# Kernel tuning notes

Measured on AMD Instinct MI355X. Metric: run time of the kernel, lower is better.

The kernel has to match this reference:

```python
import jax, jax.numpy as jnp
import numpy as np

N_NODES = 50000
N_EDGES = 1600000
IN_CH = 128
HEADS = 4
OUT_PER_HEAD = 32  # out_channels // heads with concat=True
NEG_SLOPE = 0.2    # GATConv default leaky_relu slope
SOFTMAX_EPS = 1e-16  # PyG scatter-softmax denominator eps
LN_EPS = 1e-5


def setup_inputs() -> dict:
    key = jax.random.key(0)
    ks = jax.random.split(key, 8)
    x = jax.random.normal(ks[0], (N_NODES, IN_CH), dtype=jnp.float32)
    edge_index = jax.random.randint(ks[1], (2, N_EDGES), 0, N_NODES, dtype=jnp.int32)
    W = jax.random.normal(ks[2], (IN_CH, HEADS * OUT_PER_HEAD), dtype=jnp.float32) * (1.0 / np.sqrt(IN_CH))
    att_src = jax.random.normal(ks[3], (HEADS, OUT_PER_HEAD), dtype=jnp.float32) * 0.1
    att_dst = jax.random.normal(ks[4], (HEADS, OUT_PER_HEAD), dtype=jnp.float32) * 0.1
    bias = jnp.zeros((HEADS * OUT_PER_HEAD,), dtype=jnp.float32)
    gamma = jnp.ones((HEADS * OUT_PER_HEAD,), dtype=jnp.float32)
    beta = jnp.zeros((HEADS * OUT_PER_HEAD,), dtype=jnp.float32)
    return {"x": x, "edge_index": edge_index, "W": W, "att_src": att_src,
            "att_dst": att_dst, "bias": bias, "gamma": gamma, "beta": beta}


def reference(x, edge_index, W, att_src, att_dst, bias, gamma, beta):
    N = x.shape[0]
    H, C = att_src.shape
    # GATConv default add_self_loops=True
    loop = jnp.arange(N, dtype=edge_index.dtype)
    src = jnp.concatenate([edge_index[0], loop])  # message source j
    dst = jnp.concatenate([edge_index[1], loop])  # aggregation target i

    h = (x @ W).reshape(N, H, C)                      # [N,H,C]
    a_s = jnp.einsum('nhc,hc->nh', h, att_src)        # [N,H]
    a_d = jnp.einsum('nhc,hc->nh', h, att_dst)        # [N,H]

    logits = jax.nn.leaky_relu(a_s[src] + a_d[dst], NEG_SLOPE)  # [E,H]
    # segment softmax over edges grouped by destination node
    m = jax.ops.segment_max(logits, dst, num_segments=N)        # [N,H]
    m = jnp.where(jnp.isfinite(m), m, 0.0)
    e = jnp.exp(logits - m[dst])
    s = jax.ops.segment_sum(e, dst, num_segments=N)             # [N,H]
    alpha = e / (s[dst] + SOFTMAX_EPS)                          # [E,H]

    msg = h[src] * alpha[:, :, None]                            # [E,H,C]
    out = jax.ops.segment_sum(msg, dst, num_segments=N)         # [N,H,C]
    out = out.reshape(N, H * C) + bias

    mu = out.mean(axis=-1, keepdims=True)
    var = ((out - mu) ** 2).mean(axis=-1, keepdims=True)
    y = (out - mu) / jnp.sqrt(var + LN_EPS) * gamma + beta
    return jax.nn.elu(y)
```

## Files before the change

kernel.cpp:

```cpp
#include <hip/hip_runtime.h>
#include <hip/hip_bf16.h>

typedef __hip_bfloat16 bf16;
typedef unsigned int u32;
typedef unsigned short u16;

constexpr int N   = 50000;
constexpr int E   = 1600000;
constexpr int C   = 128;
constexpr int H   = 4;
constexpr int NB  = 782;
constexpr int CAP = 2560;
constexpr int CHUNK = 4096;
constexpr float NEG  = 0.2f;
constexpr float SEPS = 1e-16f;
constexpr float LEPS = 1e-5f;

__device__ __forceinline__ float lo16(u32 v) { return __uint_as_float(v << 16); }
__device__ __forceinline__ float hi16(u32 v) { return __uint_as_float(v & 0xFFFF0000u); }

__global__ __launch_bounds__(256) void k1_gemm(
    const float* __restrict__ x, const float* __restrict__ W,
    const float* __restrict__ att_s, const float* __restrict__ att_d,
    bf16* __restrict__ hb, float* __restrict__ as_, float* __restrict__ ad_)
{
    const int nb = blockIdx.x * 16;
    const int t  = threadIdx.x;
    __shared__ float sx[16 * 128];
    const float4* xg = (const float4*)(x + nb * 128);
    ((float4*)sx)[t]       = xg[t];
    ((float4*)sx)[t + 256] = xg[t + 256];
    __syncthreads();

    const int c = t & 127;
    const int g = t >> 7;
    const float* xb = sx + (g << 10);
    float acc[8] = {0.f, 0.f, 0.f, 0.f, 0.f, 0.f, 0.f, 0.f};

    for (int k = 0; k < 128; k += 4) {
        const float w0 = W[(k + 0) * 128 + c];
        const float w1 = W[(k + 1) * 128 + c];
        const float w2 = W[(k + 2) * 128 + c];
        const float w3 = W[(k + 3) * 128 + c];
#pragma unroll
        for (int j = 0; j < 8; ++j) {
            const float4 xv = *(const float4*)(xb + j * 128 + k);
            acc[j] = fmaf(xv.x, w0, fmaf(xv.y, w1, fmaf(xv.z, w2, fmaf(xv.w, w3, acc[j]))));
        }
    }

    const int lane = t & 63;
    const int head = c >> 5;
    const float asc = att_s[c], adc = att_d[c];
#pragma unroll
    for (int j = 0; j < 8; ++j) {
        const int node = nb + (g << 3) + j;
        hb[node * 128 + c] = __float2bfloat16(acc[j]);
        float vs = acc[j] * asc;
        float vd = acc[j] * adc;
#pragma unroll
        for (int off = 16; off; off >>= 1) {
            vs += __shfl_xor(vs, off, 64);
            vd += __shfl_xor(vd, off, 64);
        }
        if ((lane & 31) == 0) {
            as_[node * H + head] = vs;
            ad_[node * H + head] = vd;
        }
    }
}

__global__ __launch_bounds__(256) void kbin(
    const int* __restrict__ ei, u32* __restrict__ gcur, u32* __restrict__ pairs)
{
    __shared__ u32 lcnt[NB], lbase[NB], lfill[NB];
    const int t = threadIdx.x;
    const int base = blockIdx.x * CHUNK;
    const int nE = min(CHUNK, E - base);
    for (int i = t; i < NB; i += 256) lcnt[i] = 0;
    __syncthreads();
    for (int i = t; i < nE; i += 256)
        atomicAdd(&lcnt[((u32)ei[E + base + i]) >> 6], 1u);
    __syncthreads();
    for (int i = t; i < NB; i += 256) {
        u32 cb = lcnt[i];
        lbase[i] = cb ? atomicAdd(&gcur[i], cb) : 0u;
        lfill[i] = 0u;
    }
    __syncthreads();
    for (int i = t; i < nE; i += 256) {
        u32 src = (u32)ei[base + i];
        u32 dst = (u32)ei[E + base + i];
        u32 b = dst >> 6;
        u32 pos = atomicAdd(&lfill[b], 1u);
        pairs[(size_t)b * CAP + lbase[b] + pos] = src | ((dst & 63u) << 16);
    }
}

__global__ __launch_bounds__(64) void kscan(
    const u32* __restrict__ gcur, u32* __restrict__ bbase, int* __restrict__ row_ptr)
{
    const int t = threadIdx.x;
    u32 vals[13];
    u32 s = 0;
#pragma unroll
    for (int i = 0; i < 13; ++i) {
        int idx = t * 13 + i;
        u32 v = (idx < NB) ? gcur[idx] : 0u;
        vals[i] = s; s += v;
    }
    u32 incl = s;
#pragma unroll
    for (int off = 1; off < 64; off <<= 1) {
        u32 u = __shfl_up(incl, off, 64);
        if (t >= off) incl += u;
    }
    const u32 excl = incl - s;
#pragma unroll
    for (int i = 0; i < 13; ++i) {
        int idx = t * 13 + i;
        if (idx < NB) bbase[idx] = excl + vals[i];
    }
    if (t == 0) row_ptr[N] = E;
}

__global__ __launch_bounds__(256) void kfill2(
    const u32* __restrict__ pairs, const u32* __restrict__ gcur,
    const u32* __restrict__ bbase, int* __restrict__ row_ptr, u16* __restrict__ col)
{
    __shared__ int jcnt[64], joff[64], jcur[64];
    const int b = blockIdx.x, t = threadIdx.x;
    const int cntb = (int)gcur[b];
    const int base = (int)bbase[b];
    if (t < 64) jcnt[t] = 0;
    __syncthreads();
    const u32* pr = pairs + (size_t)b * CAP;
    for (int i = t; i < cntb; i += 256) atomicAdd(&jcnt[pr[i] >> 16], 1);
    __syncthreads();
    if (t < 64) {
        int v = jcnt[t], incl = v;
#pragma unroll
        for (int off = 1; off < 64; off <<= 1) {
            int u = __shfl_up(incl, off, 64);
            if (t >= off) incl += u;
        }
        joff[t] = incl - v;
        const int n = b * 64 + t;
        if (n < N) row_ptr[n] = base + joff[t];
        jcur[t] = 0;
    }
    __syncthreads();
    for (int i = t; i < cntb; i += 256) {
        const u32 p = pr[i];
        const int j = p >> 16;
        const int pos = atomicAdd(&jcur[j], 1);
        col[base + joff[j] + pos] = (u16)(p & 0xFFFFu);
    }
}

__global__ __launch_bounds__(256) void kd_agg_ln(
    const int* __restrict__ row_ptr, const u16* __restrict__ col,
    const u32* __restrict__ hb, const float* __restrict__ as_,
    const float* __restrict__ ad_,
    const float* __restrict__ bias, const float* __restrict__ gamma,
    const float* __restrict__ beta, float* __restrict__ out)
{
    int gid = blockIdx.x * blockDim.x + threadIdx.x;
    int n = gid >> 6;
    if (n >= N) return;
    const int lane = gid & 63;
    const int head = lane >> 4;

    const float adn = ad_[n * H + head];
    float l = as_[n * H + head] + adn;
    l = fmaxf(l, NEG * l);
    float w = __expf(l);
    float den = w;
    u32 hv = hb[n * 64 + lane];
    float num0 = w * lo16(hv);
    float num1 = w * hi16(hv);

    int k = row_ptr[n];
    const int end = row_ptr[n + 1];
    for (; k + 4 <= end; k += 4) {
        const int s0 = col[k], s1 = col[k + 1], s2 = col[k + 2], s3 = col[k + 3];
        float l0 = as_[s0 * H + head] + adn;
        float l1 = as_[s1 * H + head] + adn;
        float l2 = as_[s2 * H + head] + adn;
        float l3 = as_[s3 * H + head] + adn;
        const u32 v0 = hb[s0 * 64 + lane];
        const u32 v1 = hb[s1 * 64 + lane];
        const u32 v2 = hb[s2 * 64 + lane];
        const u32 v3 = hb[s3 * 64 + lane];
        l0 = fmaxf(l0, NEG * l0); l1 = fmaxf(l1, NEG * l1);
        l2 = fmaxf(l2, NEG * l2); l3 = fmaxf(l3, NEG * l3);
        const float w0 = __expf(l0), w1 = __expf(l1);
        const float w2 = __expf(l2), w3 = __expf(l3);
        den += (w0 + w1) + (w2 + w3);
        num0 = fmaf(w0, lo16(v0), num0); num1 = fmaf(w0, hi16(v0), num1);
        num0 = fmaf(w1, lo16(v1), num0); num1 = fmaf(w1, hi16(v1), num1);
        num0 = fmaf(w2, lo16(v2), num0); num1 = fmaf(w2, hi16(v2), num1);
        num0 = fmaf(w3, lo16(v3), num0); num1 = fmaf(w3, hi16(v3), num1);
    }
    for (; k < end; ++k) {
        const int s = col[k];
        float ls = as_[s * H + head] + adn;
        ls = fmaxf(ls, NEG * ls);
        const float ws = __expf(ls);
        const u32 vs = hb[s * 64 + lane];
        den += ws;
        num0 = fmaf(ws, lo16(vs), num0);
        num1 = fmaf(ws, hi16(vs), num1);
    }

    const int c0 = lane * 2;
    const float inv_den = 1.f / (den + SEPS);
    float v0 = num0 * inv_den + bias[c0];
    float v1 = num1 * inv_den + bias[c0 + 1];

    float sum = v0 + v1;
#pragma unroll
    for (int off = 32; off; off >>= 1) sum += __shfl_xor(sum, off, 64);
    const float mu = sum * (1.0f / C);
    const float d0 = v0 - mu, d1 = v1 - mu;
    float sq = d0 * d0 + d1 * d1;
#pragma unroll
    for (int off = 32; off; off >>= 1) sq += __shfl_xor(sq, off, 64);
    const float inv = rsqrtf(sq * (1.0f / C) + LEPS);
    float y0 = d0 * inv * gamma[c0]     + beta[c0];
    float y1 = d1 * inv * gamma[c0 + 1] + beta[c0 + 1];
    y0 = y0 > 0.f ? y0 : __expf(y0) - 1.f;
    y1 = y1 > 0.f ? y1 : __expf(y1) - 1.f;
    float2 o; o.x = y0; o.y = y1;
    *(float2*)(out + (size_t)n * C + c0) = o;
}

extern "C" void kernel_launch(void* const* d_in, const int* in_sizes, int n_in,
                              void* d_out, int out_size, void* d_ws, size_t ws_size,
                              hipStream_t stream)
{
    const float* x     = (const float*)d_in[0];
    const int*   ei    = (const int*)  d_in[1];
    const float* W     = (const float*)d_in[2];
    const float* att_s = (const float*)d_in[3];
    const float* att_d = (const float*)d_in[4];
    const float* bias  = (const float*)d_in[5];
    const float* gamma = (const float*)d_in[6];
    const float* beta  = (const float*)d_in[7];
    float* out = (float*)d_out;

    char* p = (char*)d_ws;
    bf16*  hb      = (bf16*)p;   p += (size_t)N * C * sizeof(bf16);
    float* as_     = (float*)p;  p += (size_t)N * H * sizeof(float);
    float* ad_     = (float*)p;  p += (size_t)N * H * sizeof(float);
    u32*   pairs   = (u32*)p;    p += (size_t)NB * CAP * sizeof(u32);
    u16*   col     = (u16*)p;    p += ((size_t)E * sizeof(u16) + 15) & ~(size_t)15;
    int*   row_ptr = (int*)p;    p += ((size_t)(N + 1) * sizeof(int) + 15) & ~(size_t)15;
    u32*   gcur    = (u32*)p;    p += (size_t)NB * sizeof(u32);
    u32*   bbase   = (u32*)p;

    hipMemsetAsync(gcur, 0, NB * sizeof(u32), stream);
    k1_gemm<<<N / 16, 256, 0, stream>>>(x, W, att_s, att_d, hb, as_, ad_);
    kbin<<<(E + CHUNK - 1) / CHUNK, 256, 0, stream>>>(ei, gcur, pairs);
    kscan<<<1, 64, 0, stream>>>(gcur, bbase, row_ptr);
    kfill2<<<NB, 256, 0, stream>>>(pairs, gcur, bbase, row_ptr, col);
    kd_agg_ln<<<(N * 64) / 256, 256, 0, stream>>>(
        row_ptr, col, (const u32*)hb, as_, ad_, bias, gamma, beta, out);
}
```

Baseline: 245.3 us.

## Distribute edge weight computation across lanes in aggregation kernel

The aggregation kernel now loads 16 edge indices per head in parallel, one per lane, and computes their attention weights once per edge. The weights go through LDS and the indices are broadcast with readlane. Previously every lane of a head redundantly loaded each col index and as_ value and evaluated exp. The denominator is then reduced with a 16-lane shuffle, and bias, gamma and beta are read as float2. This adds LDS traffic and chunked inner loops, and relies on wave-synchronous behaviour for the LDS writes and reads within each wave.

Measured after the change: 239.8 us. 1.02x faster.

```diff
diff --git a/kernel.cpp b/kernel.cpp
--- a/kernel.cpp
+++ b/kernel.cpp
@@ -165,58 +165,79 @@
     const float* __restrict__ bias, const float* __restrict__ gamma,
     const float* __restrict__ beta, float* __restrict__ out)
 {
-    int gid = blockIdx.x * blockDim.x + threadIdx.x;
-    int n = gid >> 6;
+    __shared__ float wlds[4][64];
+    const int tid  = threadIdx.x;
+    const int lane = tid & 63;
+    const int wv   = __builtin_amdgcn_readfirstlane(tid >> 6);
+    const int n    = __builtin_amdgcn_readfirstlane((int)blockIdx.x * 4 + (tid >> 6));
     if (n >= N) return;
-    const int lane = gid & 63;
-    const int head = lane >> 4;
+
+    const int head  = lane >> 4;
+    const int eoff  = lane & 15;
+    const int wbase = head << 4;
+    float* __restrict__ wrow = wlds[wv];
 
     const float adn = ad_[n * H + head];
-    float l = as_[n * H + head] + adn;
-    l = fmaxf(l, NEG * l);
-    float w = __expf(l);
-    float den = w;
-    u32 hv = hb[n * 64 + lane];
-    float num0 = w * lo16(hv);
-    float num1 = w * hi16(hv);
-
-    int k = row_ptr[n];
+    const float asn = as_[n * H + head];
+
+    float ls = asn + adn;
+    ls = fmaxf(ls, NEG * ls);
+    const float wself = __expf(ls);
+    float den = (eoff == 0) ? wself : 0.f;
+    const u32 hvs = hb[n * 64 + lane];
+    float num0 = wself * lo16(hvs);
+    float num1 = wself * hi16(hvs);
+
+    const int k0  = row_ptr[n];
     const int end = row_ptr[n + 1];
-    for (; k + 4 <= end; k += 4) {
-        const int s0 = col[k], s1 = col[k + 1], s2 = col[k + 2], s3 = col[k + 3];
-        float l0 = as_[s0 * H + head] + adn;
-        float l1 = as_[s1 * H + head] + adn;
-        float l2 = as_[s2 * H + head] + adn;
-        float l3 = as_[s3 * H + head] + adn;
-        const u32 v0 = hb[s0 * 64 + lane];
-        const u32 v1 = hb[s1 * 64 + lane];
-        const u32 v2 = hb[s2 * 64 + lane];
-        const u32 v3 = hb[s3 * 64 + lane];
-        l0 = fmaxf(l0, NEG * l0); l1 = fmaxf(l1, NEG * l1);
-        l2 = fmaxf(l2, NEG * l2); l3 = fmaxf(l3, NEG * l3);
-        const float w0 = __expf(l0), w1 = __expf(l1);
-        const float w2 = __expf(l2), w3 = __expf(l3);
-        den += (w0 + w1) + (w2 + w3);
-        num0 = fmaf(w0, lo16(v0), num0); num1 = fmaf(w0, hi16(v0), num1);
-        num0 = fmaf(w1, lo16(v1), num0); num1 = fmaf(w1, hi16(v1), num1);
-        num0 = fmaf(w2, lo16(v2), num0); num1 = fmaf(w2, hi16(v2), num1);
-        num0 = fmaf(w3, lo16(v3), num0); num1 = fmaf(w3, hi16(v3), num1);
-    }
-    for (; k < end; ++k) {
-        const int s = col[k];
-        float ls = as_[s * H + head] + adn;
-        ls = fmaxf(ls, NEG * ls);
-        const float ws = __expf(ls);
-        const u32 vs = hb[s * 64 + lane];
-        den += ws;
-        num0 = fmaf(ws, lo16(vs), num0);
-        num1 = fmaf(ws, hi16(vs), num1);
-    }
+
+    for (int k = k0; k < end; k += 16) {
+        const int cnt = min(16, end - k);
+        int   colv = 0;
+        float w    = 0.f;
+        if (eoff < cnt) {
+            colv = col[k + eoff];
+            const float a = as_[colv * H + head];
+            float le = a + adn;
+            le = fmaxf(le, NEG * le);
+            w = __expf(le);
+        }
+        den += w;
+        wrow[lane] = w;
+
+        int e = 0;
+        for (; e + 4 <= cnt; e += 4) {
+            const float4 w4 = *(const float4*)(wrow + wbase + e);
+            const int s0 = __builtin_amdgcn_readlane(colv, e + 0);
+            const int s1 = __builtin_amdgcn_readlane(colv, e + 1);
+            const int s2 = __builtin_amdgcn_readlane(colv, e + 2);
+            const int s3 = __builtin_amdgcn_readlane(colv, e + 3);
+            const u32 v0 = hb[s0 * 64 + lane];
+            const u32 v1 = hb[s1 * 64 + lane];
+            const u32 v2 = hb[s2 * 64 + lane];
+            const u32 v3 = hb[s3 * 64 + lane];
+            num0 = fmaf(w4.x, lo16(v0), num0); num1 = fmaf(w4.x, hi16(v0), num1);
+            num0 = fmaf(w4.y, lo16(v1), num0); num1 = fmaf(w4.y, hi16(v1), num1);
+            num0 = fmaf(w4.z, lo16(v2), num0); num1 = fmaf(w4.z, hi16(v2), num1);
+            num0 = fmaf(w4.w, lo16(v3), num0); num1 = fmaf(w4.w, hi16(v3), num1);
+        }
+        for (; e < cnt; ++e) {
+            const float we = wrow[wbase + e];
+            const int  s  = __builtin_amdgcn_readlane(colv, e);
+            const u32  v  = hb[s * 64 + lane];
+            num0 = fmaf(we, lo16(v), num0);
+            num1 = fmaf(we, hi16(v), num1);
+        }
+    }
+
+#pragma unroll
+    for (int off = 1; off < 16; off <<= 1) den += __shfl_xor(den, off, 64);
 
     const int c0 = lane * 2;
     const float inv_den = 1.f / (den + SEPS);
-    float v0 = num0 * inv_den + bias[c0];
-    float v1 = num1 * inv_den + bias[c0 + 1];
+    const float2 bi = *(const float2*)(bias + c0);
+    float v0 = num0 * inv_den + bi.x;
+    float v1 = num1 * inv_den + bi.y;
 
     float sum = v0 + v1;
 #pragma unroll
@@ -227,8 +248,10 @@
 #pragma unroll
     for (int off = 32; off; off >>= 1) sq += __shfl_xor(sq, off, 64);
     const float inv = rsqrtf(sq * (1.0f / C) + LEPS);
-    float y0 = d0 * inv * gamma[c0]     + beta[c0];
-    float y1 = d1 * inv * gamma[c0 + 1] + beta[c0 + 1];
+    const float2 ga = *(const float2*)(gamma + c0);
+    const float2 be = *(const float2*)(beta  + c0);
+    float y0 = d0 * inv * ga.x + be.x;
+    float y1 = d1 * inv * ga.y + be.y;
     y0 = y0 > 0.f ? y0 : __expf(y0) - 1.f;
     y1 = y1 > 0.f ? y1 : __expf(y1) - 1.f;
     float2 o; o.x = y0; o.y = y1;
```
